# Performance work log

Hardware: AMD Instinct MI355X
Metric: run time of the kernel (lower is better)

Reference implementation:

```python
import jax, jax.numpy as jnp
import numpy as np


def setup_inputs() -> dict:
    key = jax.random.key(0)
    k0, k1, k2, k3 = jax.random.split(key, 4)
    B, C_IN, H, W = 8, 256, 64, 64
    O, NUM = 256, 8  # output channels, number of regions
    mat0 = jax.random.normal(k0, (B, C_IN, H, W), dtype=jnp.float32)
    mat1 = jax.random.normal(k1, (O, C_IN, NUM), dtype=jnp.float32)  # per-region 1x1 filters (shared across batch, batch_W=1)
    mask = jax.random.uniform(k2, (NUM, H, W), dtype=jnp.float32)    # soft region weights per pixel
    Alpha = jax.random.uniform(k3, (NUM,), dtype=jnp.float32)        # per-region modulation scale
    return {"mat0": mat0, "mat1": mat1, "mask": mask, "Alpha": Alpha, "use_alpha": 1, "beta": 1}


def reference(mat0, mat1, mask, Alpha, use_alpha, beta):
    # Deformable (region-aware) matmul: for each pixel (h,w), apply the
    # region-r filter mat1[:, :, r] to mat0[:, :, h, w], weighted by the
    # per-pixel soft region mask (optionally alpha-modulated per region).
    # out[b,o,h,w] = sum_r sum_c mat0[b,c,h,w] * mat1[o,c,r] * Alpha[r] * mask[r,h,w]
    m1 = mat1 * Alpha if use_alpha else mat1  # [O, C, R] scaled per region
    return jnp.einsum('bchw,ocr,rhw->bohw', mat0, m1, mask)
```

## Files before the change

kernel.cpp:

```cpp
#include <hip/hip_runtime.h>
#include <hip/hip_bf16.h>
#include <stdint.h>


typedef __attribute__((ext_vector_type(8)))  short short8;
typedef __attribute__((ext_vector_type(16))) float f32x16;

#define C_IN  256
#define HW_   4096
#define NRND  32

__device__ __forceinline__ short f2bf(float x) {
  union { __hip_bfloat16 h; short s; } u;
  u.h = __float2bfloat16(x);
  return u.s;
}

__global__ __launch_bounds__(256) void prep_w_kernel(
    const float* __restrict__ mat1, const float* __restrict__ Alpha,
    const int* __restrict__ use_alpha, short* __restrict__ Aprep) {
  int t = blockIdx.x * 256 + threadIdx.x;
  int o = t & 255;
  int c = t >> 8;
  int ua = use_alpha[0];
  const float* src = mat1 + ((size_t)o * C_IN + c) * 8;
  short8 v;
#pragma unroll
  for (int r = 0; r < 8; ++r) {
    float s = ua ? Alpha[r] : 1.0f;
    v[r] = f2bf(src[r] * s);
  }
  *(short8*)(Aprep + ((size_t)c * 256 + o) * 8) = v;
}

__global__ __launch_bounds__(512, 4) void gemm_deform_kernel(
    const float* __restrict__ mat0, const short* __restrict__ Aprep,
    const float* __restrict__ mask, float* __restrict__ out) {
  int bid = blockIdx.x;
  int wg = (bid & 7) * 64 + (bid >> 3);
  int tile_m = wg & 1;
  int tile_n = wg >> 1;
  int o0 = tile_m * 128;
  int n0 = tile_n * 128;
  int b  = n0 >> 12;
  int p0 = n0 & 4095;

  int t    = threadIdx.x;
  int lane = t & 63;
  int w    = t >> 6;
  int wc   = w & 3;
  int wr   = w >> 2;
  int l31  = lane & 31;
  int cr   = lane >> 5;

  int col = p0 + wc * 32 + l31;
  float mk[8];
#pragma unroll
  for (int r = 0; r < 8; ++r) mk[r] = mask[r * HW_ + col];

  const short8* __restrict__ Ap = (const short8*)Aprep;
  int aoff = cr * 256 + o0 + wr * 64 + l31;

  const float* __restrict__ m0b =
      mat0 + ((size_t)b * C_IN + cr) * HW_ + col;

  f32x16 acc[2];
#pragma unroll
  for (int mi = 0; mi < 2; ++mi)
#pragma unroll
    for (int j = 0; j < 16; ++j) acc[mi][j] = 0.f;

  short8 af[4][2];
  float  P[4];

#pragma unroll
  for (int kq = 0; kq < 4; ++kq) {
#pragma unroll
    for (int mi = 0; mi < 2; ++mi)
      af[kq][mi] = Ap[aoff + kq * 512 + mi * 32];
    P[kq] = m0b[(size_t)(kq * 2) * HW_];
  }

#pragma unroll 1
  for (int rd = 0; rd < NRND - 1; ++rd) {
    int abase = (rd + 1) * 2048 + aoff;
    const float* mnext = m0b + (size_t)((rd + 1) * 8) * HW_;
#pragma unroll
    for (int kq = 0; kq < 4; ++kq) {
      short8 bv;
#pragma unroll
      for (int r = 0; r < 8; ++r) bv[r] = f2bf(P[kq] * mk[r]);
      acc[0] = __builtin_amdgcn_mfma_f32_32x32x16_bf16(af[kq][0], bv, acc[0], 0, 0, 0);
      acc[1] = __builtin_amdgcn_mfma_f32_32x32x16_bf16(af[kq][1], bv, acc[1], 0, 0, 0);
      af[kq][0] = Ap[abase + kq * 512];
      af[kq][1] = Ap[abase + kq * 512 + 32];
      P[kq] = mnext[(size_t)(kq * 2) * HW_];
    }
  }
#pragma unroll
  for (int kq = 0; kq < 4; ++kq) {
    short8 bv;
#pragma unroll
    for (int r = 0; r < 8; ++r) bv[r] = f2bf(P[kq] * mk[r]);
    acc[0] = __builtin_amdgcn_mfma_f32_32x32x16_bf16(af[kq][0], bv, acc[0], 0, 0, 0);
    acc[1] = __builtin_amdgcn_mfma_f32_32x32x16_bf16(af[kq][1], bv, acc[1], 0, 0, 0);
  }

  size_t obase = (size_t)b * 256 * HW_ + col;
#pragma unroll
  for (int mi = 0; mi < 2; ++mi) {
#pragma unroll
    for (int reg = 0; reg < 16; ++reg) {
      int row = o0 + wr * 64 + mi * 32 + (reg & 3) + 8 * (reg >> 2) + 4 * cr;
      out[obase + (size_t)row * HW_] = acc[mi][reg];
    }
  }
}

extern "C" void kernel_launch(void* const* d_in, const int* in_sizes, int n_in,
                              void* d_out, int out_size, void* d_ws, size_t ws_size,
                              hipStream_t stream) {
  const float* mat0      = (const float*)d_in[0];
  const float* mat1      = (const float*)d_in[1];
  const float* mask      = (const float*)d_in[2];
  const float* Alpha     = (const float*)d_in[3];
  const int*   use_alpha = (const int*)d_in[4];
  (void)in_sizes; (void)n_in; (void)out_size; (void)ws_size;

  short* Aprep = (short*)d_ws;
  float* outp  = (float*)d_out;

  prep_w_kernel<<<256, 256, 0, stream>>>(mat1, Alpha, use_alpha, Aprep);
  gemm_deform_kernel<<<512, 512, 0, stream>>>(mat0, Aprep, mask, outp);
}
```

Before: 57.41 us.

## Stage weights through double-buffered LDS and give each wave a 2x2 MFMA tile

The workgroup drops from 512 to 256 threads, and each wave now computes a 64x64 output tile (2x2 MFMAs) instead of 64x32. This reuses each A fragment across two B columns. Weight fragments are no longer loaded from global memory per wave; they are copied asynchronously into double-buffered LDS with global_load_lds and shared across waves, with barriers between rounds. This is meant to cut redundant global weight traffic and raise MFMA work per load, at the cost of fewer waves per CU, added synchronisation and more registers per thread.

```diff
diff --git a/kernel.cpp b/kernel.cpp
--- a/kernel.cpp
+++ b/kernel.cpp
@@ -33,9 +33,11 @@
   *(short8*)(Aprep + ((size_t)c * 256 + o) * 8) = v;
 }
 
-__global__ __launch_bounds__(512, 4) void gemm_deform_kernel(
+__global__ __launch_bounds__(256, 2) void gemm_deform_kernel(
     const float* __restrict__ mat0, const short* __restrict__ Aprep,
     const float* __restrict__ mask, float* __restrict__ out) {
+  __shared__ short8 A_lds[2][1024];
+
   int bid = blockIdx.x;
   int wg = (bid & 7) * 64 + (bid >> 3);
   int tile_m = wg & 1;
@@ -48,71 +50,105 @@
   int t    = threadIdx.x;
   int lane = t & 63;
   int w    = t >> 6;
-  int wc   = w & 3;
-  int wr   = w >> 2;
+  int wc   = w & 1;
+  int wr   = w >> 1;
   int l31  = lane & 31;
   int cr   = lane >> 5;
 
-  int col = p0 + wc * 32 + l31;
-  float mk[8];
+  int colb = p0 + wc * 64 + l31;
+  float mk[2][8];
 #pragma unroll
-  for (int r = 0; r < 8; ++r) mk[r] = mask[r * HW_ + col];
-
-  const short8* __restrict__ Ap = (const short8*)Aprep;
-  int aoff = cr * 256 + o0 + wr * 64 + l31;
+  for (int ni = 0; ni < 2; ++ni)
+#pragma unroll
+    for (int r = 0; r < 8; ++r)
+      mk[ni][r] = mask[r * HW_ + colb + ni * 32];
 
   const float* __restrict__ m0b =
-      mat0 + ((size_t)b * C_IN + cr) * HW_ + col;
+      mat0 + ((size_t)b * C_IN + cr) * HW_ + colb;
 
-  f32x16 acc[2];
+  const __attribute__((address_space(1))) uint32_t* gA =
+      (const __attribute__((address_space(1))) uint32_t*)Aprep;
+  int soo  = (w & 1) * 64 + lane;
+  int scqb = w >> 1;
+
+  f32x16 acc[2][2];
 #pragma unroll
   for (int mi = 0; mi < 2; ++mi)
 #pragma unroll
-    for (int j = 0; j < 16; ++j) acc[mi][j] = 0.f;
+    for (int ni = 0; ni < 2; ++ni)
+#pragma unroll
+      for (int j = 0; j < 16; ++j) acc[mi][ni][j] = 0.f;
 
-  short8 af[4][2];
-  float  P[4];
+  float P0[4][2], P1[4][2];
 
+  auto STAGE = [&](int rd, int buf) {
+    __attribute__((address_space(3))) uint32_t* lA =
+        (__attribute__((address_space(3))) uint32_t*)&A_lds[buf][0];
 #pragma unroll
-  for (int kq = 0; kq < 4; ++kq) {
+    for (int i = 0; i < 4; ++i) {
+      int gslot = (rd * 8 + i * 2 + scqb) * 256 + o0 + soo;
+      __builtin_amdgcn_global_load_lds(gA + (size_t)gslot * 4,
+                                       lA + (size_t)(i * 256 + w * 64) * 4,
+                                       16, 0, 0);
+    }
+  };
+
+  auto LOADP = [&](float (&P)[4][2], int rd) {
+    const float* mp = m0b + (size_t)(rd * 8) * HW_;
 #pragma unroll
-    for (int mi = 0; mi < 2; ++mi)
-      af[kq][mi] = Ap[aoff + kq * 512 + mi * 32];
-    P[kq] = m0b[(size_t)(kq * 2) * HW_];
+    for (int kq = 0; kq < 4; ++kq) {
+      P[kq][0] = mp[(size_t)(kq * 2) * HW_];
+      P[kq][1] = mp[(size_t)(kq * 2) * HW_ + 32];
+    }
+  };
+
+  auto COMP = [&](const short8* __restrict__ Abuf, float (&P)[4][2], int rd) {
+    int rp = rd + 2 > 31 ? 31 : rd + 2;
+    const float* mnext = m0b + (size_t)(rp * 8) * HW_;
+#pragma unroll
+    for (int kq = 0; kq < 4; ++kq) {
+      short8 a0 = Abuf[(kq * 2 + cr) * 128 + wr * 64 + l31];
+      short8 a1 = Abuf[(kq * 2 + cr) * 128 + wr * 64 + 32 + l31];
+      short8 bv0, bv1;
+#pragma unroll
+      for (int r = 0; r < 8; ++r) {
+        bv0[r] = f2bf(P[kq][0] * mk[0][r]);
+        bv1[r] = f2bf(P[kq][1] * mk[1][r]);
+      }
+      acc[0][0] = __builtin_amdgcn_mfma_f32_32x32x16_bf16(a0, bv0, acc[0][0], 0, 0, 0);
+      acc[0][1] = __builtin_amdgcn_mfma_f32_32x32x16_bf16(a0, bv1, acc[0][1], 0, 0, 0);
+      acc[1][0] = __builtin_amdgcn_mfma_f32_32x32x16_bf16(a1, bv0, acc[1][0], 0, 0, 0);
+      acc[1][1] = __builtin_amdgcn_mfma_f32_32x32x16_bf16(a1, bv1, acc[1][1], 0, 0, 0);
+      P[kq][0] = mnext[(size_t)(kq * 2) * HW_];
+      P[kq][1] = mnext[(size_t)(kq * 2) * HW_ + 32];
+    }
+  };
+
+  STAGE(0, 0);
+  LOADP(P0, 0);
+  LOADP(P1, 1);
+  __syncthreads();
+
+#pragma unroll 1
+  for (int rd = 0; rd < NRND; rd += 2) {
+    STAGE(rd + 1, 1);
+    COMP(&A_lds[0][0], P0, rd);
+    __syncthreads();
+    if (rd + 2 < NRND) STAGE(rd + 2, 0);
+    COMP(&A_lds[1][0], P1, rd + 1);
+    __syncthreads();
   }
 
-#pragma unroll 1
-  for (int rd = 0; rd < NRND - 1; ++rd) {
-    int abase = (rd + 1) * 2048 + aoff;
-    const float* mnext = m0b + (size_t)((rd + 1) * 8) * HW_;
-#pragma unroll
-    for (int kq = 0; kq < 4; ++kq) {
-      short8 bv;
-#pragma unroll
-      for (int r = 0; r < 8; ++r) bv[r] = f2bf(P[kq] * mk[r]);
-      acc[0] = __builtin_amdgcn_mfma_f32_32x32x16_bf16(af[kq][0], bv, acc[0], 0, 0, 0);
-      acc[1] = __builtin_amdgcn_mfma_f32_32x32x16_bf16(af[kq][1], bv, acc[1], 0, 0, 0);
-      af[kq][0] = Ap[abase + kq * 512];
-      af[kq][1] = Ap[abase + kq * 512 + 32];
-      P[kq] = mnext[(size_t)(kq * 2) * HW_];
-    }
-  }
-#pragma unroll
-  for (int kq = 0; kq < 4; ++kq) {
-    short8 bv;
-#pragma unroll
-    for (int r = 0; r < 8; ++r) bv[r] = f2bf(P[kq] * mk[r]);
-    acc[0] = __builtin_amdgcn_mfma_f32_32x32x16_bf16(af[kq][0], bv, acc[0], 0, 0, 0);
-    acc[1] = __builtin_amdgcn_mfma_f32_32x32x16_bf16(af[kq][1], bv, acc[1], 0, 0, 0);
-  }
-
-  size_t obase = (size_t)b * 256 * HW_ + col;
+  size_t obase = (size_t)b * 256 * HW_ + colb;
 #pragma unroll
   for (int mi = 0; mi < 2; ++mi) {
 #pragma unroll
-    for (int reg = 0; reg < 16; ++reg) {
-      int row = o0 + wr * 64 + mi * 32 + (reg & 3) + 8 * (reg >> 2) + 4 * cr;
-      out[obase + (size_t)row * HW_] = acc[mi][reg];
+    for (int ni = 0; ni < 2; ++ni) {
+#pragma unroll
+      for (int reg = 0; reg < 16; ++reg) {
+        int row = o0 + wr * 64 + mi * 32 + (reg & 3) + 8 * (reg >> 2) + 4 * cr;
+        out[obase + (size_t)row * HW_ + ni * 32] = acc[mi][ni][reg];
+      }
     }
   }
 }
@@ -131,5 +167,5 @@
   float* outp  = (float*)d_out;
 
   prep_w_kernel<<<256, 256, 0, stream>>>(mat1, Alpha, use_alpha, Aprep);
-  gemm_deform_kernel<<<512, 512, 0, stream>>>(mat0, Aprep, mask, outp);
+  gemm_deform_kernel<<<512, 256, 0, stream>>>(mat0, Aprep, mask, outp);
 }
```

New measurement: 53.30 us. -7.2%, faster.
